# Performance work log

Measured on AMD Instinct MI355X. Metric: run time of the kernel, lower is better.

The kernel has to match this reference:

```python
import jax, jax.numpy as jnp
import numpy as np

NUM_QUANTIZERS = 8


def setup_inputs() -> dict:
    key = jax.random.key(0)
    k1, k2 = jax.random.split(key)
    B, W, C = 16, 2048, 512
    Q, K = NUM_QUANTIZERS, 1024
    x = jax.random.normal(k1, (B, W, C), dtype=jnp.float32)
    # per-stage codebooks (shared_codebook=False), xavier-normal-ish scale
    codebooks = jax.random.normal(k2, (Q, K, C), dtype=jnp.float32) * (2.0 / (K + C)) ** 0.5
    return {"x": x, "codebooks": codebooks}


def reference(x, codebooks):
    """Residual quantization: per-stage cdist+argmin+lookup+residual update.

    x: [B, W, C] encoder latents; codebooks: [Q, K, C].
    Returns (final_z_q [B*W, C], commitment_loss scalar) — final_z_q is
    sum over quantizer stages of the straight-through quantized outputs
    (is_train=True path).
    """
    B, W, C = x.shape
    first_z_e = x.reshape(B * W, C)            # (b w) c
    z_e = first_z_e
    z_d = jnp.zeros_like(first_z_e)
    quant_sum = jnp.zeros_like(first_z_e)
    q_latent = jnp.float32(0.0)
    e_latent = jnp.float32(0.0)
    rq_latent = jnp.float32(0.0)
    for i in range(codebooks.shape[0]):
        cb = codebooks[i]                      # [K, C]
        # squared euclidean distances (argmin-equivalent to torch.cdist)
        dist2 = (jnp.sum(z_e * z_e, axis=1, keepdims=True)
                 - 2.0 * (z_e @ cb.T)
                 + jnp.sum(cb * cb, axis=1))   # [N, K]
        idx = jnp.argmin(dist2, axis=1)        # [N]
        z_q = cb[idx]                          # codebook lookup, [N, C]
        z_d = z_d + jax.lax.stop_gradient(z_q)
        q_latent = q_latent + jnp.mean((jax.lax.stop_gradient(z_e) - z_q) ** 2)
        e_latent = e_latent + jnp.mean((z_e - jax.lax.stop_gradient(z_q)) ** 2)
        rq_latent = rq_latent + jnp.mean((first_z_e - z_d) ** 2)
        # straight-through estimator (is_train=True)
        z_q_st = z_e + jax.lax.stop_gradient(z_q - z_e)
        quant_sum = quant_sum + z_q_st
        z_e = z_e - z_q_st
    commitment_loss = 0.75 * q_latent + e_latent + rq_latent
    return quant_sum, commitment_loss
```

## Files before the change

### kernel.cpp

```cpp
#include <hip/hip_runtime.h>

#define N_ROWS 32768
#define C_DIM  512
#define K_CODES 1024
#define Q_STAGES 8

typedef __attribute__((ext_vector_type(8))) short bf16x8;
typedef __attribute__((ext_vector_type(4))) float f32x4;
typedef __attribute__((ext_vector_type(4))) unsigned short u16x4;
typedef __attribute__((ext_vector_type(8))) unsigned short u16x8;

#define ZEH_OFF 0ull
#define ZEL_OFF 33554432ull
#define CBH_OFF 67108864ull
#define CBL_OFF 68157440ull
#define C2_OFF  69206016ull
#define IDX_OFF 69238784ull
#define RPT_OFF 69304320ull
#define LSB_OFF 69312512ull

#define GLD(gp, lp) __builtin_amdgcn_global_load_lds( \
    (const __attribute__((address_space(1))) void*)(gp), \
    (__attribute__((address_space(3))) void*)(lp), 16, 0, 0)

__device__ __forceinline__ float bf_hi_f(float f) {
    return __uint_as_float(__float_as_uint(f) & 0xFFFF0000u);
}
__device__ __forceinline__ unsigned short bf_hi_u(float f) {
    return (unsigned short)(__float_as_uint(f) >> 16);
}
__device__ __forceinline__ float u2f(unsigned short u) {
    return __uint_as_float(((unsigned int)u) << 16);
}

__global__ __launch_bounds__(256) void split_kernel(
    const float* __restrict__ src, unsigned short* __restrict__ h,
    unsigned short* __restrict__ l, int n4)
{
    int i = blockIdx.x * 256 + threadIdx.x;
    if (i >= n4) return;
    float4 v = *(const float4*)(src + (size_t)i * 4);
    u16x4 hv, lv;
    float f, hf;
    f = v.x; hv[0] = bf_hi_u(f); hf = bf_hi_f(f); lv[0] = bf_hi_u(f - hf);
    f = v.y; hv[1] = bf_hi_u(f); hf = bf_hi_f(f); lv[1] = bf_hi_u(f - hf);
    f = v.z; hv[2] = bf_hi_u(f); hf = bf_hi_f(f); lv[2] = bf_hi_u(f - hf);
    f = v.w; hv[3] = bf_hi_u(f); hf = bf_hi_f(f); lv[3] = bf_hi_u(f - hf);
    *(u16x4*)(h + (size_t)i * 4) = hv;
    *(u16x4*)(l + (size_t)i * 4) = lv;
}

__global__ __launch_bounds__(256) void rowsq_kernel(
    const float* __restrict__ src, float* __restrict__ dst, int nrows)
{
    int wave = (blockIdx.x * blockDim.x + threadIdx.x) >> 6;
    int lane = threadIdx.x & 63;
    if (wave >= nrows) return;
    const float* p = src + (size_t)wave * C_DIM + lane * 8;
    float4 a = *(const float4*)p;
    float4 b = *(const float4*)(p + 4);
    float s = a.x*a.x + a.y*a.y + a.z*a.z + a.w*a.w
            + b.x*b.x + b.y*b.y + b.z*b.z + b.w*b.w;
    #pragma unroll
    for (int off = 1; off < 64; off <<= 1) s += __shfl_xor(s, off);
    if (lane == 0) dst[wave] = s;
}

#define DBM2 128
#define DBNC 256
#define DBK 32
#define NSTEPS 64

__global__ __launch_bounds__(512, 2) void dist_kernel(
    const unsigned short* __restrict__ zeh, const unsigned short* __restrict__ zel,
    const unsigned short* __restrict__ cbh, const unsigned short* __restrict__ cbl,
    const float* __restrict__ c2s, unsigned short* __restrict__ idx_out)
{
    __shared__ unsigned short sA[3][2][DBM2 * DBK];
    __shared__ unsigned short sB[3][2][DBNC * DBK];
    __shared__ float c2_lds[K_CODES];

    const int tid  = threadIdx.x;
    const int lane = tid & 63;
    const int w    = tid >> 6;
    const int wr   = w >> 2;
    const int wc   = w & 3;
    const int lr   = lane & 15;
    const int kg   = lane >> 4;
    const int row0 = blockIdx.x * DBM2;

    for (int i = tid; i < K_CODES; i += 512) c2_lds[i] = c2s[i];

    const int srow = lane >> 2;
    const int scol = (((lane & 3) ^ ((srow >> 1) & 3))) * 8;
    const int aslot = (kg ^ ((lr >> 1) & 3)) * 8;

    float rbv[4][4];
    int   rbi[4][4];
    #pragma unroll
    for (int i = 0; i < 4; ++i)
        #pragma unroll
        for (int r = 0; r < 4; ++r) { rbv[i][r] = 3.4e38f; rbi[i][r] = 0x7fffffff; }

    f32x4 acc[4][4];
    #pragma unroll
    for (int i = 0; i < 4; ++i)
        #pragma unroll
        for (int j = 0; j < 4; ++j) acc[i][j] = (f32x4)0.f;

    auto stage = [&](int t, int b) {
        const int col0 = (t >> 4) * DBNC;
        const int kk = (t & 15) * DBK;
        GLD(zeh + (size_t)(row0 + w * 16 + srow) * C_DIM + kk + scol,
            &sA[b][0][(w * 16) * DBK]);
        GLD(zel + (size_t)(row0 + w * 16 + srow) * C_DIM + kk + scol,
            &sA[b][1][(w * 16) * DBK]);
        #pragma unroll
        for (int u = 0; u < 2; ++u) {
            const int rB = w * 32 + u * 16;
            GLD(cbh + (size_t)(col0 + rB + srow) * C_DIM + kk + scol,
                &sB[b][0][rB * DBK]);
            GLD(cbl + (size_t)(col0 + rB + srow) * C_DIM + kk + scol,
                &sB[b][1][rB * DBK]);
        }
    };

    __syncthreads();
    stage(0, 0);
    stage(1, 1);

    int cur = 0;
    #pragma unroll 1
    for (int t = 0; t < NSTEPS; ++t) {
        if (t == NSTEPS - 1) {
            asm volatile("s_waitcnt vmcnt(0)" ::: "memory");
        } else {
            asm volatile("s_waitcnt vmcnt(6)" ::: "memory");
        }
        __builtin_amdgcn_s_barrier();

        bf16x8 ah[4], al[4], bh[4], bl[4];
        #pragma unroll
        for (int mi = 0; mi < 4; ++mi) {
            const int rowoff = (wr * 64 + mi * 16 + lr) * DBK + aslot;
            ah[mi] = *(const bf16x8*)&sA[cur][0][rowoff];
            al[mi] = *(const bf16x8*)&sA[cur][1][rowoff];
        }
        #pragma unroll
        for (int ni = 0; ni < 4; ++ni) {
            const int rowoff = (wc * 64 + ni * 16 + lr) * DBK + aslot;
            bh[ni] = *(const bf16x8*)&sB[cur][0][rowoff];
            bl[ni] = *(const bf16x8*)&sB[cur][1][rowoff];
        }

        if (t < NSTEPS - 2) {
            int nxt = cur + 2; if (nxt > 2) nxt -= 3;
            stage(t + 2, nxt);
        }

        __builtin_amdgcn_s_setprio(1);
        #pragma unroll
        for (int mi = 0; mi < 4; ++mi)
            #pragma unroll
            for (int ni = 0; ni < 4; ++ni)
                acc[mi][ni] = __builtin_amdgcn_mfma_f32_16x16x32_bf16(
                    ah[mi], bh[ni], acc[mi][ni], 0, 0, 0);
        #pragma unroll
        for (int mi = 0; mi < 4; ++mi)
            #pragma unroll
            for (int ni = 0; ni < 4; ++ni)
                acc[mi][ni] = __builtin_amdgcn_mfma_f32_16x16x32_bf16(
                    ah[mi], bl[ni], acc[mi][ni], 0, 0, 0);
        #pragma unroll
        for (int mi = 0; mi < 4; ++mi)
            #pragma unroll
            for (int ni = 0; ni < 4; ++ni)
                acc[mi][ni] = __builtin_amdgcn_mfma_f32_16x16x32_bf16(
                    al[mi], bh[ni], acc[mi][ni], 0, 0, 0);
        __builtin_amdgcn_s_setprio(0);

        if ((t & 15) == 15) {
            const int col0 = (t >> 4) * DBNC;
            #pragma unroll
            for (int ni = 0; ni < 4; ++ni) {
                const int code = col0 + wc * 64 + ni * 16 + lr;
                const float c2v = c2_lds[code];
                #pragma unroll
                for (int mi = 0; mi < 4; ++mi)
                    #pragma unroll
                    for (int r = 0; r < 4; ++r) {
                        float d = fmaf(-2.f, acc[mi][ni][r], c2v);
                        if (d < rbv[mi][r]) { rbv[mi][r] = d; rbi[mi][r] = code; }
                    }
            }
            #pragma unroll
            for (int i = 0; i < 4; ++i)
                #pragma unroll
                for (int j = 0; j < 4; ++j) acc[i][j] = (f32x4)0.f;
        }

        cur = (cur == 2) ? 0 : cur + 1;
    }

    #pragma unroll
    for (int off = 1; off < 16; off <<= 1) {
        #pragma unroll
        for (int mi = 0; mi < 4; ++mi)
            #pragma unroll
            for (int r = 0; r < 4; ++r) {
                float ov = __shfl_xor(rbv[mi][r], off);
                int   oi = __shfl_xor(rbi[mi][r], off);
                if (ov < rbv[mi][r] || (ov == rbv[mi][r] && oi < rbi[mi][r])) {
                    rbv[mi][r] = ov; rbi[mi][r] = oi;
                }
            }
    }

    __syncthreads();
    float (*s_v)[4] = (float (*)[4])&sA[0][0][0];
    int   (*s_i)[4] = (int (*)[4])((char*)&sA[0][0][0] + DBM2 * 4 * 4);
    if (lr == 0) {
        #pragma unroll
        for (int mi = 0; mi < 4; ++mi)
            #pragma unroll
            for (int r = 0; r < 4; ++r) {
                int lrow = wr * 64 + mi * 16 + kg * 4 + r;
                s_v[lrow][wc] = rbv[mi][r];
                s_i[lrow][wc] = rbi[mi][r];
            }
    }
    __syncthreads();
    if (tid < DBM2) {
        float bv = s_v[tid][0]; int bi = s_i[tid][0];
        #pragma unroll
        for (int c = 1; c < 4; ++c) {
            float v = s_v[tid][c]; int i = s_i[tid][c];
            if (v < bv || (v == bv && i < bi)) { bv = v; bi = i; }
        }
        idx_out[row0 + tid] = (unsigned short)bi;
    }
}

__global__ __launch_bounds__(1024) void update_kernel(
    const int s, const float* __restrict__ x, const float* __restrict__ cb,
    const unsigned short* __restrict__ idx_sel, float* __restrict__ out,
    unsigned short* __restrict__ zeh, unsigned short* __restrict__ zel,
    float* __restrict__ rpart)
{
    __shared__ float swsum[16];
    const int wid = threadIdx.x >> 6, lane = threadIdx.x & 63;
    const int r = blockIdx.x * 16 + wid;
    const int bi = idx_sel[r];
    const size_t base = (size_t)r * C_DIM + lane * 8;
    const float* q = cb + (size_t)bi * C_DIM + lane * 8;

    float4 q0 = *(const float4*)q;
    float4 q1 = *(const float4*)(q + 4);
    float qq[8] = {q0.x, q0.y, q0.z, q0.w, q1.x, q1.y, q1.z, q1.w};

    float v[8];
    if (s == 0) {
        float4 z0 = *(const float4*)(x + base);
        float4 z1 = *(const float4*)(x + base + 4);
        v[0]=z0.x; v[1]=z0.y; v[2]=z0.z; v[3]=z0.w;
        v[4]=z1.x; v[5]=z1.y; v[6]=z1.z; v[7]=z1.w;
    } else {
        u16x8 h = *(const u16x8*)(zeh + base);
        u16x8 l = *(const u16x8*)(zel + base);
        #pragma unroll
        for (int j = 0; j < 8; ++j) v[j] = u2f(h[j]) + u2f(l[j]);
    }

    float rr[8];
    #pragma unroll
    for (int j = 0; j < 8; ++j) rr[j] = v[j] - qq[j];

    if (s < Q_STAGES - 1) {
        u16x8 hh, ll;
        #pragma unroll
        for (int j = 0; j < 8; ++j) {
            hh[j] = bf_hi_u(rr[j]);
            float lo = rr[j] - bf_hi_f(rr[j]);
            ll[j] = bf_hi_u(lo);
        }
        *(u16x8*)(zeh + base) = hh;
        *(u16x8*)(zel + base) = ll;
    } else {
        float4 x0 = *(const float4*)(x + base);
        float4 x1 = *(const float4*)(x + base + 4);
        float4 o0, o1;
        o0.x = x0.x - rr[0]; o0.y = x0.y - rr[1];
        o0.z = x0.z - rr[2]; o0.w = x0.w - rr[3];
        o1.x = x1.x - rr[4]; o1.y = x1.y - rr[5];
        o1.z = x1.z - rr[6]; o1.w = x1.w - rr[7];
        *(float4*)(out + base)     = o0;
        *(float4*)(out + base + 4) = o1;
    }

    float ssum = 0.f;
    #pragma unroll
    for (int j = 0; j < 8; ++j) ssum += rr[j] * rr[j];
    #pragma unroll
    for (int off = 1; off < 64; off <<= 1) ssum += __shfl_xor(ssum, off);
    if (lane == 0) swsum[wid] = ssum;
    __syncthreads();
    if (threadIdx.x == 0) {
        float t = 0.f;
        #pragma unroll
        for (int i = 0; i < 16; ++i) t += swsum[i];
        rpart[blockIdx.x] = t;
    }
}

__global__ __launch_bounds__(1024) void reduce2048_kernel(
    const float* __restrict__ rpart, float* __restrict__ slot)
{
    __shared__ float sm[1024];
    int t = threadIdx.x;
    sm[t] = rpart[t] + rpart[t + 1024];
    __syncthreads();
    for (int w2 = 512; w2 > 0; w2 >>= 1) {
        if (t < w2) sm[t] += sm[t + w2];
        __syncthreads();
    }
    if (t == 0) *slot = sm[0];
}

__global__ void finalize_kernel(const float* __restrict__ lossbuf,
                                float* __restrict__ out)
{
    if (threadIdx.x == 0) {
        float s = 0.f;
        #pragma unroll
        for (int i = 0; i < Q_STAGES; ++i) s += lossbuf[i];
        out[0] = 2.75f * s / (float)((size_t)N_ROWS * C_DIM);
    }
}

extern "C" void kernel_launch(void* const* d_in, const int* in_sizes, int n_in,
                              void* d_out, int out_size, void* d_ws, size_t ws_size,
                              hipStream_t stream)
{
    const float* x   = (const float*)d_in[0];
    const float* cbs = (const float*)d_in[1];
    float* out = (float*)d_out;
    char* ws = (char*)d_ws;

    unsigned short* zeh = (unsigned short*)(ws + ZEH_OFF);
    unsigned short* zel = (unsigned short*)(ws + ZEL_OFF);
    unsigned short* cbh = (unsigned short*)(ws + CBH_OFF);
    unsigned short* cbl = (unsigned short*)(ws + CBL_OFF);
    float* c2    = (float*)(ws + C2_OFF);
    unsigned short* gidx = (unsigned short*)(ws + IDX_OFF);
    float* rpart = (float*)(ws + RPT_OFF);
    float* lossb = (float*)(ws + LSB_OFF);

    split_kernel<<<(N_ROWS * C_DIM / 4 + 255) / 256, 256, 0, stream>>>(
        x, zeh, zel, N_ROWS * C_DIM / 4);
    rowsq_kernel<<<(Q_STAGES * K_CODES * 64) / 256, 256, 0, stream>>>(
        cbs, c2, Q_STAGES * K_CODES);

    for (int s = 0; s < Q_STAGES; ++s) {
        const float* cb = cbs + (size_t)s * K_CODES * C_DIM;
        split_kernel<<<(K_CODES * C_DIM / 4 + 255) / 256, 256, 0, stream>>>(
            cb, cbh, cbl, K_CODES * C_DIM / 4);
        dist_kernel<<<N_ROWS / DBM2, 512, 0, stream>>>(
            zeh, zel, cbh, cbl, c2 + (size_t)s * K_CODES, gidx);
        update_kernel<<<N_ROWS / 16, 1024, 0, stream>>>(
            s, x, cb, gidx, out, zeh, zel, rpart);
        reduce2048_kernel<<<1, 1024, 0, stream>>>(rpart, lossb + s);
    }
    finalize_kernel<<<1, 64, 0, stream>>>(lossb, out + (size_t)N_ROWS * C_DIM);
}
```

Measured before the change: 1.012 ms.

## Fuse residual update into distance kernel and merge loss reductions

```diff
diff --git a/kernel.cpp b/kernel.cpp
--- a/kernel.cpp
+++ b/kernel.cpp
@@ -15,9 +15,7 @@
 #define CBH_OFF 67108864ull
 #define CBL_OFF 68157440ull
 #define C2_OFF  69206016ull
-#define IDX_OFF 69238784ull
-#define RPT_OFF 69304320ull
-#define LSB_OFF 69312512ull
+#define RPT_OFF 69238784ull
 
 #define GLD(gp, lp) __builtin_amdgcn_global_load_lds( \
     (const __attribute__((address_space(1))) void*)(gp), \
@@ -71,14 +69,18 @@
 #define DBK 32
 #define NSTEPS 64
 
-__global__ __launch_bounds__(512, 2) void dist_kernel(
-    const unsigned short* __restrict__ zeh, const unsigned short* __restrict__ zel,
+__global__ __launch_bounds__(512, 2) void dist_fused_kernel(
+    const int s, const float* __restrict__ x,
+    unsigned short* __restrict__ zeh, unsigned short* __restrict__ zel,
     const unsigned short* __restrict__ cbh, const unsigned short* __restrict__ cbl,
-    const float* __restrict__ c2s, unsigned short* __restrict__ idx_out)
+    const float* __restrict__ cbf, const float* __restrict__ c2s,
+    float* __restrict__ out, float* __restrict__ rpart)
 {
     __shared__ unsigned short sA[3][2][DBM2 * DBK];
     __shared__ unsigned short sB[3][2][DBNC * DBK];
     __shared__ float c2_lds[K_CODES];
+    __shared__ int   win[DBM2];
+    __shared__ float swsum[8];
 
     const int tid  = threadIdx.x;
     const int lane = tid & 63;
@@ -237,104 +239,91 @@
             float v = s_v[tid][c]; int i = s_i[tid][c];
             if (v < bv || (v == bv && i < bi)) { bv = v; bi = i; }
         }
-        idx_out[row0 + tid] = (unsigned short)bi;
-    }
-}
-
-__global__ __launch_bounds__(1024) void update_kernel(
-    const int s, const float* __restrict__ x, const float* __restrict__ cb,
-    const unsigned short* __restrict__ idx_sel, float* __restrict__ out,
-    unsigned short* __restrict__ zeh, unsigned short* __restrict__ zel,
-    float* __restrict__ rpart)
-{
-    __shared__ float swsum[16];
-    const int wid = threadIdx.x >> 6, lane = threadIdx.x & 63;
-    const int r = blockIdx.x * 16 + wid;
-    const int bi = idx_sel[r];
-    const size_t base = (size_t)r * C_DIM + lane * 8;
-    const float* q = cb + (size_t)bi * C_DIM + lane * 8;
-
-    float4 q0 = *(const float4*)q;
-    float4 q1 = *(const float4*)(q + 4);
-    float qq[8] = {q0.x, q0.y, q0.z, q0.w, q1.x, q1.y, q1.z, q1.w};
-
-    float v[8];
-    if (s == 0) {
-        float4 z0 = *(const float4*)(x + base);
-        float4 z1 = *(const float4*)(x + base + 4);
-        v[0]=z0.x; v[1]=z0.y; v[2]=z0.z; v[3]=z0.w;
-        v[4]=z1.x; v[5]=z1.y; v[6]=z1.z; v[7]=z1.w;
-    } else {
-        u16x8 h = *(const u16x8*)(zeh + base);
-        u16x8 l = *(const u16x8*)(zel + base);
-        #pragma unroll
-        for (int j = 0; j < 8; ++j) v[j] = u2f(h[j]) + u2f(l[j]);
-    }
-
-    float rr[8];
-    #pragma unroll
-    for (int j = 0; j < 8; ++j) rr[j] = v[j] - qq[j];
-
-    if (s < Q_STAGES - 1) {
-        u16x8 hh, ll;
-        #pragma unroll
-        for (int j = 0; j < 8; ++j) {
-            hh[j] = bf_hi_u(rr[j]);
-            float lo = rr[j] - bf_hi_f(rr[j]);
-            ll[j] = bf_hi_u(lo);
-        }
-        *(u16x8*)(zeh + base) = hh;
-        *(u16x8*)(zel + base) = ll;
-    } else {
-        float4 x0 = *(const float4*)(x + base);
-        float4 x1 = *(const float4*)(x + base + 4);
-        float4 o0, o1;
-        o0.x = x0.x - rr[0]; o0.y = x0.y - rr[1];
-        o0.z = x0.z - rr[2]; o0.w = x0.w - rr[3];
-        o1.x = x1.x - rr[4]; o1.y = x1.y - rr[5];
-        o1.z = x1.z - rr[6]; o1.w = x1.w - rr[7];
-        *(float4*)(out + base)     = o0;
-        *(float4*)(out + base + 4) = o1;
-    }
-
+        win[tid] = bi;
+    }
+    __syncthreads();
+
+    const int lane8 = lane * 8;
     float ssum = 0.f;
-    #pragma unroll
-    for (int j = 0; j < 8; ++j) ssum += rr[j] * rr[j];
+    #pragma unroll 1
+    for (int j = 0; j < 16; ++j) {
+        const int lrow = w * 16 + j;
+        const size_t base = (size_t)(row0 + lrow) * C_DIM + lane8;
+        const int bi = win[lrow];
+        const float* q = cbf + (size_t)bi * C_DIM + lane8;
+        float4 q0 = *(const float4*)q;
+        float4 q1 = *(const float4*)(q + 4);
+        float qq[8] = {q0.x, q0.y, q0.z, q0.w, q1.x, q1.y, q1.z, q1.w};
+
+        float v[8];
+        if (s == 0) {
+            float4 z0 = *(const float4*)(x + base);
+            float4 z1 = *(const float4*)(x + base + 4);
+            v[0]=z0.x; v[1]=z0.y; v[2]=z0.z; v[3]=z0.w;
+            v[4]=z1.x; v[5]=z1.y; v[6]=z1.z; v[7]=z1.w;
+        } else {
+            u16x8 h = *(const u16x8*)(zeh + base);
+            u16x8 l = *(const u16x8*)(zel + base);
+            #pragma unroll
+            for (int e = 0; e < 8; ++e) v[e] = u2f(h[e]) + u2f(l[e]);
+        }
+
+        float rr[8];
+        #pragma unroll
+        for (int e = 0; e < 8; ++e) rr[e] = v[e] - qq[e];
+
+        if (s < Q_STAGES - 1) {
+            u16x8 hh, ll;
+            #pragma unroll
+            for (int e = 0; e < 8; ++e) {
+                hh[e] = bf_hi_u(rr[e]);
+                float lo = rr[e] - bf_hi_f(rr[e]);
+                ll[e] = bf_hi_u(lo);
+            }
+            *(u16x8*)(zeh + base) = hh;
+            *(u16x8*)(zel + base) = ll;
+        } else {
+            float4 x0 = *(const float4*)(x + base);
+            float4 x1 = *(const float4*)(x + base + 4);
+            float4 o0, o1;
+            o0.x = x0.x - rr[0]; o0.y = x0.y - rr[1];
+            o0.z = x0.z - rr[2]; o0.w = x0.w - rr[3];
+            o1.x = x1.x - rr[4]; o1.y = x1.y - rr[5];
+            o1.z = x1.z - rr[6]; o1.w = x1.w - rr[7];
+            *(float4*)(out + base)     = o0;
+            *(float4*)(out + base + 4) = o1;
+        }
+
+        #pragma unroll
+        for (int e = 0; e < 8; ++e) ssum += rr[e] * rr[e];
+    }
     #pragma unroll
     for (int off = 1; off < 64; off <<= 1) ssum += __shfl_xor(ssum, off);
-    if (lane == 0) swsum[wid] = ssum;
-    __syncthreads();
-    if (threadIdx.x == 0) {
-        float t = 0.f;
-        #pragma unroll
-        for (int i = 0; i < 16; ++i) t += swsum[i];
-        rpart[blockIdx.x] = t;
-    }
-}
-
-__global__ __launch_bounds__(1024) void reduce2048_kernel(
-    const float* __restrict__ rpart, float* __restrict__ slot)
-{
-    __shared__ float sm[1024];
-    int t = threadIdx.x;
-    sm[t] = rpart[t] + rpart[t + 1024];
-    __syncthreads();
-    for (int w2 = 512; w2 > 0; w2 >>= 1) {
+    if (lane == 0) swsum[w] = ssum;
+    __syncthreads();
+    if (tid == 0) {
+        float tot = 0.f;
+        #pragma unroll
+        for (int i = 0; i < 8; ++i) tot += swsum[i];
+        rpart[blockIdx.x] = tot;
+    }
+}
+
+__global__ __launch_bounds__(256) void finalize_kernel(
+    const float* __restrict__ rpart, float* __restrict__ out_loss)
+{
+    __shared__ float sm[256];
+    const int t = threadIdx.x;
+    float v = 0.f;
+    #pragma unroll
+    for (int s = 0; s < Q_STAGES; ++s) v += rpart[s * 256 + t];
+    sm[t] = v;
+    __syncthreads();
+    for (int w2 = 128; w2 > 0; w2 >>= 1) {
         if (t < w2) sm[t] += sm[t + w2];
         __syncthreads();
     }
-    if (t == 0) *slot = sm[0];
-}
-
-__global__ void finalize_kernel(const float* __restrict__ lossbuf,
-                                float* __restrict__ out)
-{
-    if (threadIdx.x == 0) {
-        float s = 0.f;
-        #pragma unroll
-        for (int i = 0; i < Q_STAGES; ++i) s += lossbuf[i];
-        out[0] = 2.75f * s / (float)((size_t)N_ROWS * C_DIM);
-    }
+    if (t == 0) out_loss[0] = 2.75f * sm[0] / (float)((size_t)N_ROWS * C_DIM);
 }
 
 extern "C" void kernel_launch(void* const* d_in, const int* in_sizes, int n_in,
@@ -351,24 +340,24 @@
     unsigned short* cbh = (unsigned short*)(ws + CBH_OFF);
     unsigned short* cbl = (unsigned short*)(ws + CBL_OFF);
     float* c2    = (float*)(ws + C2_OFF);
-    unsigned short* gidx = (unsigned short*)(ws + IDX_OFF);
     float* rpart = (float*)(ws + RPT_OFF);
-    float* lossb = (float*)(ws + LSB_OFF);
 
     split_kernel<<<(N_ROWS * C_DIM / 4 + 255) / 256, 256, 0, stream>>>(
         x, zeh, zel, N_ROWS * C_DIM / 4);
+    split_kernel<<<(K_CODES * C_DIM / 4 + 255) / 256, 256, 0, stream>>>(
+        cbs, cbh, cbl, K_CODES * C_DIM / 4);
     rowsq_kernel<<<(Q_STAGES * K_CODES * 64) / 256, 256, 0, stream>>>(
         cbs, c2, Q_STAGES * K_CODES);
 
     for (int s = 0; s < Q_STAGES; ++s) {
-        const float* cb = cbs + (size_t)s * K_CODES * C_DIM;
-        split_kernel<<<(K_CODES * C_DIM / 4 + 255) / 256, 256, 0, stream>>>(
-            cb, cbh, cbl, K_CODES * C_DIM / 4);
-        dist_kernel<<<N_ROWS / DBM2, 512, 0, stream>>>(
-            zeh, zel, cbh, cbl, c2 + (size_t)s * K_CODES, gidx);
-        update_kernel<<<N_ROWS / 16, 1024, 0, stream>>>(
-            s, x, cb, gidx, out, zeh, zel, rpart);
-        reduce2048_kernel<<<1, 1024, 0, stream>>>(rpart, lossb + s);
-    }
-    finalize_kernel<<<1, 64, 0, stream>>>(lossb, out + (size_t)N_ROWS * C_DIM);
-}
+        const float* cbf = cbs + (size_t)s * K_CODES * C_DIM;
+        dist_fused_kernel<<<N_ROWS / DBM2, 512, 0, stream>>>(
+            s, x, zeh, zel, cbh, cbl, cbf, c2 + (size_t)s * K_CODES,
+            out, rpart + s * 256);
+        if (s < Q_STAGES - 1) {
+            split_kernel<<<(K_CODES * C_DIM / 4 + 255) / 256, 256, 0, stream>>>(
+                cbf + (size_t)K_CODES * C_DIM, cbh, cbl, K_CODES * C_DIM / 4);
+        }
+    }
+    finalize_kernel<<<1, 256, 0, stream>>>(rpart, out + (size_t)N_ROWS * C_DIM);
+}
```

Result: faster. 968.1 us (-4.4%).
